# Kernel tuning notes

Hardware: AMD Instinct MI355X
Metric: run time of the kernel (lower is better)

## Reference

```python
import jax, jax.numpy as jnp
import numpy as np

SEQ, IN, H = 64, 100000, 50


def setup_inputs() -> dict:
    key = jax.random.key(0)
    k0, k1, k2, k3, k4 = jax.random.split(key, 5)
    x = jax.random.normal(k0, (SEQ, 1, IN), dtype=jnp.float32) * 0.02
    Wi = jax.random.normal(k1, (IN, 4 * H), dtype=jnp.float32) * 0.01
    bi = jax.random.normal(k2, (4 * H,), dtype=jnp.float32) * 0.01
    Wh = jax.random.normal(k3, (H, 4 * H), dtype=jnp.float32) * 0.1
    bh = jax.random.normal(k4, (4 * H,), dtype=jnp.float32) * 0.01
    return {"x": x, "Wi": Wi, "bi": bi, "Wh": Wh, "bh": bh}


def reference(x, Wi, bi, Wh, bh):
    # x: [seq, batch=1, input_size] -- each row is a flattened ParameterList.
    # Precompute the input projection for all steps at once (one big GEMM),
    # same math as per-step input_weights(input) since it has no recurrence.
    gates_in = jnp.einsum('sbi,ig->sbg', x, Wi) + bi + bh  # [seq, 1, 4H]

    def step(carry, g_in):
        hx, cx = carry
        gates = g_in + hx @ Wh  # [1, 4H]
        i, f, g, o = jnp.split(gates, 4, axis=1)
        i = jax.nn.sigmoid(i)
        f = jax.nn.sigmoid(f)
        g = jnp.tanh(g)
        o = jax.nn.sigmoid(o)
        cy = f * cx + i * g
        hy = o * jnp.tanh(cy)
        return (hy, cy), None

    h0 = jnp.zeros((1, H), dtype=x.dtype)
    c0 = jnp.zeros((1, H), dtype=x.dtype)
    (h_final, _), _ = jax.lax.scan(step, (h0, c0), gates_in)
    # torch.squeeze(out_hidden): (1, H) -> (H,)
    return jnp.squeeze(h_final)
```

## Files before the change

### kernel.cpp

```cpp
#include <hip/hip_runtime.h>
#include <hip/hip_bf16.h>


#define K_DIM 100000
#define NG 200
#define NS 64
#define TK 32
#define NBLK 256
#define NTILES 3125
#define CELLS (NS * NG)
#define CELLS4 (CELLS / 4)
#define ROWU 40
#define K2BLKS (CELLS4 / 16)

typedef unsigned short u16;
typedef unsigned int   u32;
typedef __bf16 bf16x8 __attribute__((ext_vector_type(8)));
typedef float  f32x16 __attribute__((ext_vector_type(16)));

static __device__ __forceinline__ u32 rne16(float f) {
    u32 u = __float_as_uint(f);
    return (u + 0x7FFFu + ((u >> 16) & 1u)) >> 16;
}
static __device__ __forceinline__ void split_hl(float f, u32& h, u32& l) {
    u32 u  = __float_as_uint(f);
    u32 hb = u & 0xFFFF0000u;
    h = hb >> 16;
    l = rne16(f - __uint_as_float(hb));
}
static __device__ __forceinline__ void split4(float4 v, u32 h[4], u32 l[4]) {
    split_hl(v.x, h[0], l[0]); split_hl(v.y, h[1], l[1]);
    split_hl(v.z, h[2], l[2]); split_hl(v.w, h[3], l[3]);
}
static __device__ __forceinline__ f32x16 mfma_bf(uint4 a, uint4 b, f32x16 c) {
    return __builtin_amdgcn_mfma_f32_32x32x16_bf16(
        __builtin_bit_cast(bf16x8, a), __builtin_bit_cast(bf16x8, b), c, 0, 0, 0);
}

__global__ __launch_bounds__(512, 1) void k1_gemm_partial(
    const float* __restrict__ x, const float* __restrict__ Wi,
    float* __restrict__ partial, unsigned int* __restrict__ ticket)
{
    __shared__ __align__(16) u16 WH[2][224 * ROWU];
    __shared__ __align__(16) u16 WL[2][224 * ROWU];
    __shared__ __align__(16) u16 XH[2][64 * ROWU];
    __shared__ __align__(16) u16 XL[2][64 * ROWU];

    const int t    = threadIdx.x;
    const int lane = t & 63;
    const int wave = t >> 6;
    const int m    = lane & 31;
    const int h    = lane >> 5;
    const int stile = wave >> 2;
    const int gset  = wave & 3;

    if (blockIdx.x == 0 && t == 0) *ticket = 0u;

#pragma unroll
    for (int b = 0; b < 2; ++b) {
        u32* zh = (u32*)&WH[b][200 * ROWU];
        u32* zl = (u32*)&WL[b][200 * ROWU];
        for (int i = t; i < 24 * ROWU / 2; i += 512) { zh[i] = 0; zl[i] = 0; }
    }

    const int a_g4 = t >> 3;
    const int a_k4 = t & 7;
    const bool has_w = (t < 400);
    const int xs0 = t >> 3, xk0 = t & 7;

    auto do_loads = [&](int ti, float4 (&wr)[4], float4& xr) {
        const size_t kt = (size_t)ti * TK;
        if (has_w) {
#pragma unroll
            for (int j = 0; j < 4; ++j)
                wr[j] = *(const float4*)(Wi + (kt + a_k4 * 4 + j) * NG + a_g4 * 4);
        }
        xr = *(const float4*)(x + (size_t)xs0 * K_DIM + kt + xk0 * 4);
    };
    auto stage_wi = [&](const float4 (&r)[4], u16* WHp, u16* WLp) {
        u32 hw[4][4], lw[4][4];
#pragma unroll
        for (int j = 0; j < 4; ++j) split4(r[j], hw[j], lw[j]);
#pragma unroll
        for (int j2 = 0; j2 < 4; ++j2) {
            int off = (4 * a_g4 + j2) * ROWU + a_k4 * 4;
            *(uint2*)&WHp[off] = make_uint2(hw[0][j2] | (hw[1][j2] << 16),
                                            hw[2][j2] | (hw[3][j2] << 16));
            *(uint2*)&WLp[off] = make_uint2(lw[0][j2] | (lw[1][j2] << 16),
                                            lw[2][j2] | (lw[3][j2] << 16));
        }
    };
    auto stage_x = [&](float4 v, u16* XHp, u16* XLp) {
        u32 hh[4], ll[4];
        split4(v, hh, ll);
        int off = xs0 * ROWU + xk0 * 4;
        *(uint2*)&XHp[off] = make_uint2(hh[0] | (hh[1] << 16), hh[2] | (hh[3] << 16));
        *(uint2*)&XLp[off] = make_uint2(ll[0] | (ll[1] << 16), ll[2] | (ll[3] << 16));
    };

    f32x16 acc[2];
#pragma unroll
    for (int tt = 0; tt < 2; ++tt)
#pragma unroll
        for (int r = 0; r < 16; ++r) acc[tt][r] = 0.f;

    const int aoff = (stile * 32 + m) * ROWU + h * 8;
    int boff[2];
#pragma unroll
    for (int tt = 0; tt < 2; ++tt) {
        int gt = (gset == 3 && tt == 1) ? 6 : (2 * gset + tt);
        boff[tt] = (gt * 32 + m) * ROWU + h * 8;
    }

    auto mfma_phase = [&](int p) {
        const u16* WHp = WH[p]; const u16* WLp = WL[p];
        const u16* XHp = XH[p]; const u16* XLp = XL[p];
#pragma unroll
        for (int kk = 0; kk < 2; ++kk) {
            uint4 ah = *(const uint4*)&XHp[aoff + kk * 16];
            uint4 al = *(const uint4*)&XLp[aoff + kk * 16];
#pragma unroll
            for (int tt = 0; tt < 2; ++tt) {
                uint4 bh = *(const uint4*)&WHp[boff[tt] + kk * 16];
                uint4 bl = *(const uint4*)&WLp[boff[tt] + kk * 16];
                acc[tt] = mfma_bf(ah, bh, acc[tt]);
                acc[tt] = mfma_bf(ah, bl, acc[tt]);
                acc[tt] = mfma_bf(al, bh, acc[tt]);
            }
        }
    };

    float4 waA[4], waB[4];
    float4 xaA, xaB;
    const int ti0 = blockIdx.x;
    do_loads(ti0,            waA, xaA);
    do_loads(ti0 + NBLK,     waB, xaB);
    if (has_w) stage_wi(waA, WH[0], WL[0]);
    stage_x(xaA, XH[0], XL[0]);
    do_loads(ti0 + 2 * NBLK, waA, xaA);
    __syncthreads();

    int p = 0;
    int ti = ti0;
    while (ti < NTILES) {
        {
            int tn = ti + NBLK;
            if (tn < NTILES) {
                if (has_w) stage_wi(waB, WH[p ^ 1], WL[p ^ 1]);
                stage_x(xaB, XH[p ^ 1], XL[p ^ 1]);
                int tf = tn + 2 * NBLK;
                if (tf < NTILES) do_loads(tf, waB, xaB);
            }
            mfma_phase(p);
            __syncthreads();
            p ^= 1; ti += NBLK;
        }
        if (ti >= NTILES) break;
        {
            int tn = ti + NBLK;
            if (tn < NTILES) {
                if (has_w) stage_wi(waA, WH[p ^ 1], WL[p ^ 1]);
                stage_x(xaA, XH[p ^ 1], XL[p ^ 1]);
                int tf = tn + 2 * NBLK;
                if (tf < NTILES) do_loads(tf, waA, xaA);
            }
            mfma_phase(p);
            __syncthreads();
            p ^= 1; ti += NBLK;
        }
    }

    float* base = partial + (size_t)blockIdx.x * CELLS;
#pragma unroll
    for (int tt = 0; tt < 2; ++tt) {
        if (gset == 3 && tt == 1) continue;
        int g = (2 * gset + tt) * 32 + m;
        if (g < NG) {
#pragma unroll
            for (int r = 0; r < 16; ++r) {
                int srow = stile * 32 + (r & 3) + 8 * (r >> 2) + 4 * h;
                base[srow * NG + g] = acc[tt][r];
            }
        }
    }
}

__global__ __launch_bounds__(512) void k23_reduce_lstm(
    const float* __restrict__ partial, const float* __restrict__ bi,
    const float* __restrict__ bh, float* __restrict__ gates,
    unsigned int* __restrict__ ticket,
    const float* __restrict__ Wh, float* __restrict__ out)
{
    __shared__ float4 red[512];
    const int tid   = threadIdx.x;
    const int fid   = tid & 15;
    const int slice = tid >> 4;
    const int g4    = blockIdx.x * 16 + fid;

    const float4* p4 = (const float4*)partial;
    float4 sum = make_float4(0.f, 0.f, 0.f, 0.f);
#pragma unroll 4
    for (int b = slice * 8; b < slice * 8 + 8; ++b) {
        float4 v = p4[(size_t)b * CELLS4 + g4];
        sum.x += v.x; sum.y += v.y; sum.z += v.z; sum.w += v.w;
    }
    red[tid] = sum;
    __syncthreads();
    if (tid < 16) {
        float4 tot = red[tid];
#pragma unroll
        for (int p = 1; p < 32; ++p) {
            float4 v = red[p * 16 + tid];
            tot.x += v.x; tot.y += v.y; tot.z += v.z; tot.w += v.w;
        }
        int gg = (g4 * 4) % NG;
        float4 b1 = *(const float4*)(bi + gg);
        float4 b2 = *(const float4*)(bh + gg);
        tot.x += b1.x + b2.x; tot.y += b1.y + b2.y;
        tot.z += b1.z + b2.z; tot.w += b1.w + b2.w;
        ((float4*)gates)[g4] = tot;
    }

    __shared__ unsigned int lastFlag;
    __syncthreads();
    if (tid == 0) {
        __threadfence();
        unsigned int old = atomicAdd(ticket, 1u);
        lastFlag = (old == (unsigned)(gridDim.x - 1)) ? 1u : 0u;
    }
    __syncthreads();
    if (!lastFlag) return;
    __threadfence();

    __shared__ __align__(16) float gz[CELLS];
    __shared__ float hbuf[8][64];
    __shared__ float act[2][NG];
    const int g    = tid;
    const int w    = tid >> 6;
    const int lane = tid & 63;

    {
        float4* gz4 = (float4*)gz;
        const float4* gp4 = (const float4*)gates;
        for (int i = tid; i < CELLS4; i += 512) gz4[i] = gp4[i];
    }
    float wh[50];
    if (g < NG) {
#pragma unroll
        for (int j = 0; j < 50; ++j) wh[j] = Wh[j * NG + g];
    }
    hbuf[w][lane] = 0.f;
    float c = 0.f, h = 0.f;
    const bool is_cell_gate = (g >= 100 && g < 150);
    __syncthreads();

    const float* hl = hbuf[w];
    for (int s = 0; s < 64; ++s) {
        if (g < NG) {
            float a0 = gz[s * NG + g], a1 = 0.f, a2 = 0.f, a3 = 0.f;
#pragma unroll
            for (int jj = 0; jj < 48; jj += 4) {
                float4 h4 = *(const float4*)(hl + jj);
                a0 = fmaf(h4.x, wh[jj],     a0);
                a1 = fmaf(h4.y, wh[jj + 1], a1);
                a2 = fmaf(h4.z, wh[jj + 2], a2);
                a3 = fmaf(h4.w, wh[jj + 3], a3);
            }
            {
                float2 h2 = *(const float2*)(hl + 48);
                a0 = fmaf(h2.x, wh[48], a0);
                a1 = fmaf(h2.y, wh[49], a1);
            }
            float z = (a0 + a1) + (a2 + a3);
            float e   = __expf(-z);
            float sig = 1.f / (1.f + e);
            float e2  = e * e;
            float th  = (1.f - e2) / (1.f + e2);
            act[s & 1][g] = is_cell_gate ? th : sig;
        }
        __syncthreads();
        if (lane < 50) {
            float iv = act[s & 1][lane];
            float fv = act[s & 1][50 + lane];
            float gv = act[s & 1][100 + lane];
            float ov = act[s & 1][150 + lane];
            c = fmaf(fv, c, iv * gv);
            float e2c = __expf(-2.f * c);
            h = ov * (1.f - e2c) / (1.f + e2c);
            hbuf[w][lane] = h;
        }
    }
    if (tid < 50) out[tid] = h;
}

extern "C" void kernel_launch(void* const* d_in, const int* in_sizes, int n_in,
                              void* d_out, int out_size, void* d_ws, size_t ws_size,
                              hipStream_t stream)
{
    const float* x  = (const float*)d_in[0];
    const float* Wi = (const float*)d_in[1];
    const float* bi = (const float*)d_in[2];
    const float* Wh = (const float*)d_in[3];
    const float* bh = (const float*)d_in[4];
    float* out = (float*)d_out;

    float* partial = (float*)d_ws;
    float* gates   = partial + (size_t)NBLK * CELLS;
    unsigned int* ticket = (unsigned int*)(gates + CELLS);

    k1_gemm_partial<<<NBLK, 512, 0, stream>>>(x, Wi, partial, ticket);
    k23_reduce_lstm<<<K2BLKS, 512, 0, stream>>>(partial, bi, bh, gates,
                                                ticket, Wh, out);
}
```

Before: 192.7 us.

## Run LSTM recurrence in a single wave with readlane broadcast, lighter GEMM barriers

The serial 64-step recurrence tail now runs in one wavefront: each lane owns one hidden unit and computes all four gates, with h broadcast through readlane instead of shared memory and __syncthreads per step. Gate inputs are prefetched from global one step ahead, and Wh columns are held in 200 registers per lane, with a waves_per_eu hint to allow the register budget. Separately, the GEMM tile loop replaces __syncthreads with an explicit lgkmcnt wait plus s_barrier and a sched_barrier. The tail trades block-wide parallelism for per-lane serial FMAs (200 per hidden element per step) and carries register-pressure and spill risk.

```diff
diff --git a/kernel.cpp b/kernel.cpp
--- a/kernel.cpp
+++ b/kernel.cpp
@@ -18,6 +18,12 @@
 typedef __bf16 bf16x8 __attribute__((ext_vector_type(8)));
 typedef float  f32x16 __attribute__((ext_vector_type(16)));
 
+#define TILE_BARRIER() do {                                   \
+    asm volatile("s_waitcnt lgkmcnt(0)" ::: "memory");        \
+    __builtin_amdgcn_s_barrier();                             \
+    __builtin_amdgcn_sched_barrier(0);                        \
+} while (0)
+
 static __device__ __forceinline__ u32 rne16(float f) {
     u32 u = __float_as_uint(f);
     return (u + 0x7FFFu + ((u >> 16) & 1u)) >> 16;
@@ -35,6 +41,9 @@
 static __device__ __forceinline__ f32x16 mfma_bf(uint4 a, uint4 b, f32x16 c) {
     return __builtin_amdgcn_mfma_f32_32x32x16_bf16(
         __builtin_bit_cast(bf16x8, a), __builtin_bit_cast(bf16x8, b), c, 0, 0, 0);
+}
+static __device__ __forceinline__ float rl(float v, int j) {
+    return __int_as_float(__builtin_amdgcn_readlane(__float_as_int(v), j));
 }
 
 __global__ __launch_bounds__(512, 1) void k1_gemm_partial(
@@ -138,7 +147,7 @@
     if (has_w) stage_wi(waA, WH[0], WL[0]);
     stage_x(xaA, XH[0], XL[0]);
     do_loads(ti0 + 2 * NBLK, waA, xaA);
-    __syncthreads();
+    TILE_BARRIER();
 
     int p = 0;
     int ti = ti0;
@@ -152,7 +161,7 @@
                 if (tf < NTILES) do_loads(tf, waB, xaB);
             }
             mfma_phase(p);
-            __syncthreads();
+            TILE_BARRIER();
             p ^= 1; ti += NBLK;
         }
         if (ti >= NTILES) break;
@@ -165,7 +174,7 @@
                 if (tf < NTILES) do_loads(tf, waA, xaA);
             }
             mfma_phase(p);
-            __syncthreads();
+            TILE_BARRIER();
             p ^= 1; ti += NBLK;
         }
     }
@@ -185,7 +194,9 @@
     }
 }
 
-__global__ __launch_bounds__(512) void k23_reduce_lstm(
+__global__ __launch_bounds__(512)
+__attribute__((amdgpu_waves_per_eu(2, 2)))
+void k23_reduce_lstm(
     const float* __restrict__ partial, const float* __restrict__ bi,
     const float* __restrict__ bh, float* __restrict__ gates,
     unsigned int* __restrict__ ticket,
@@ -232,65 +243,73 @@
     if (!lastFlag) return;
     __threadfence();
 
-    __shared__ __align__(16) float gz[CELLS];
-    __shared__ float hbuf[8][64];
-    __shared__ float act[2][NG];
-    const int g    = tid;
-    const int w    = tid >> 6;
-    const int lane = tid & 63;
-
+    if (tid >= 64) return;
+    const int  l  = tid;
+    const bool al = (l < 50);
+    const int  lc = al ? l : 49;
+
+    float wI[50], wF[50], wG[50], wO[50];
     {
-        float4* gz4 = (float4*)gz;
-        const float4* gp4 = (const float4*)gates;
-        for (int i = tid; i < CELLS4; i += 512) gz4[i] = gp4[i];
-    }
-    float wh[50];
-    if (g < NG) {
-#pragma unroll
-        for (int j = 0; j < 50; ++j) wh[j] = Wh[j * NG + g];
-    }
-    hbuf[w][lane] = 0.f;
+        const float* Wp = Wh + lc;
+#pragma unroll
+        for (int j = 0; j < 50; ++j) {
+            const float* r = Wp + j * NG;
+            wI[j] = r[0]; wF[j] = r[50]; wG[j] = r[100]; wO[j] = r[150];
+        }
+    }
+    const float* gp = gates + lc;
+    float gI = gp[0], gF = gp[50], gG = gp[100], gO = gp[150];
     float c = 0.f, h = 0.f;
-    const bool is_cell_gate = (g >= 100 && g < 150);
-    __syncthreads();
-
-    const float* hl = hbuf[w];
+
     for (int s = 0; s < 64; ++s) {
-        if (g < NG) {
-            float a0 = gz[s * NG + g], a1 = 0.f, a2 = 0.f, a3 = 0.f;
-#pragma unroll
-            for (int jj = 0; jj < 48; jj += 4) {
-                float4 h4 = *(const float4*)(hl + jj);
-                a0 = fmaf(h4.x, wh[jj],     a0);
-                a1 = fmaf(h4.y, wh[jj + 1], a1);
-                a2 = fmaf(h4.z, wh[jj + 2], a2);
-                a3 = fmaf(h4.w, wh[jj + 3], a3);
-            }
-            {
-                float2 h2 = *(const float2*)(hl + 48);
-                a0 = fmaf(h2.x, wh[48], a0);
-                a1 = fmaf(h2.y, wh[49], a1);
-            }
-            float z = (a0 + a1) + (a2 + a3);
-            float e   = __expf(-z);
-            float sig = 1.f / (1.f + e);
-            float e2  = e * e;
-            float th  = (1.f - e2) / (1.f + e2);
-            act[s & 1][g] = is_cell_gate ? th : sig;
-        }
-        __syncthreads();
-        if (lane < 50) {
-            float iv = act[s & 1][lane];
-            float fv = act[s & 1][50 + lane];
-            float gv = act[s & 1][100 + lane];
-            float ov = act[s & 1][150 + lane];
-            c = fmaf(fv, c, iv * gv);
-            float e2c = __expf(-2.f * c);
-            h = ov * (1.f - e2c) / (1.f + e2c);
-            hbuf[w][lane] = h;
-        }
-    }
-    if (tid < 50) out[tid] = h;
+        float nI = 0.f, nF = 0.f, nG = 0.f, nO = 0.f;
+        if (s < 63) {
+            const float* gn = gp + (s + 1) * NG;
+            nI = gn[0]; nF = gn[50]; nG = gn[100]; nO = gn[150];
+        }
+
+        float aI0 = gI, aI1 = 0.f, aI2 = 0.f, aI3 = 0.f;
+        float aF0 = gF, aF1 = 0.f, aF2 = 0.f, aF3 = 0.f;
+        float aG0 = gG, aG1 = 0.f, aG2 = 0.f, aG3 = 0.f;
+        float aO0 = gO, aO1 = 0.f, aO2 = 0.f, aO3 = 0.f;
+#pragma unroll
+        for (int j = 0; j < 48; j += 4) {
+            float h0 = rl(h, j),     h1 = rl(h, j + 1);
+            float h2 = rl(h, j + 2), h3 = rl(h, j + 3);
+            aI0 = fmaf(h0, wI[j], aI0);     aI1 = fmaf(h1, wI[j + 1], aI1);
+            aI2 = fmaf(h2, wI[j + 2], aI2); aI3 = fmaf(h3, wI[j + 3], aI3);
+            aF0 = fmaf(h0, wF[j], aF0);     aF1 = fmaf(h1, wF[j + 1], aF1);
+            aF2 = fmaf(h2, wF[j + 2], aF2); aF3 = fmaf(h3, wF[j + 3], aF3);
+            aG0 = fmaf(h0, wG[j], aG0);     aG1 = fmaf(h1, wG[j + 1], aG1);
+            aG2 = fmaf(h2, wG[j + 2], aG2); aG3 = fmaf(h3, wG[j + 3], aG3);
+            aO0 = fmaf(h0, wO[j], aO0);     aO1 = fmaf(h1, wO[j + 1], aO1);
+            aO2 = fmaf(h2, wO[j + 2], aO2); aO3 = fmaf(h3, wO[j + 3], aO3);
+        }
+        {
+            float h48 = rl(h, 48), h49 = rl(h, 49);
+            aI0 = fmaf(h48, wI[48], aI0); aI1 = fmaf(h49, wI[49], aI1);
+            aF0 = fmaf(h48, wF[48], aF0); aF1 = fmaf(h49, wF[49], aF1);
+            aG0 = fmaf(h48, wG[48], aG0); aG1 = fmaf(h49, wG[49], aG1);
+            aO0 = fmaf(h48, wO[48], aO0); aO1 = fmaf(h49, wO[49], aO1);
+        }
+        float zI = (aI0 + aI1) + (aI2 + aI3);
+        float zF = (aF0 + aF1) + (aF2 + aF3);
+        float zG = (aG0 + aG1) + (aG2 + aG3);
+        float zO = (aO0 + aO1) + (aO2 + aO3);
+
+        float eI = __expf(-zI); float iv = 1.f / (1.f + eI);
+        float eF = __expf(-zF); float fv = 1.f / (1.f + eF);
+        float eG = __expf(-zG); float e2G = eG * eG;
+        float gv = (1.f - e2G) / (1.f + e2G);
+        float eO = __expf(-zO); float ov = 1.f / (1.f + eO);
+
+        c = fmaf(fv, c, iv * gv);
+        float e2c = __expf(-2.f * c);
+        h = ov * (1.f - e2c) / (1.f + e2c);
+
+        gI = nI; gF = nF; gG = nG; gO = nO;
+    }
+    if (al) out[l] = h;
 }
 
 extern "C" void kernel_launch(void* const* d_in, const int* in_sizes, int n_in,
```

Result: slower. 206.1 us (+7.0%).
